# Optimization experiments

Measured on AMD Instinct MI355X. Metric: run time of the kernel, lower is better.

The kernel has to match this reference:

```python
import jax, jax.numpy as jnp
import numpy as np
from jax import lax

FPS_NUM = 512
GROUP_NUM = 32
RADIUS = 0.2
BIG = 1e10


def setup_inputs() -> dict:
    key = jax.random.key(0)
    k1, k2 = jax.random.split(key)
    B, N = 8, 32768
    xyz = jax.random.normal(k1, (B, N, 3), dtype=jnp.float32)
    farthest_init = jax.random.randint(k2, (B,), 0, N, dtype=jnp.int32)
    return {"xyz": xyz, "farthest_init": farthest_init}


def _fps(xyz, farthest_init):
    # xyz: [B, N, 3] -> centroids [B, FPS_NUM] int32
    B, N, _ = xyz.shape
    batch_ix = jnp.arange(B)

    def step(carry, _):
        distance, farthest = carry          # [B,N], [B]
        centroid = xyz[batch_ix, farthest]  # [B,3]
        dist = jnp.sum((xyz - centroid[:, None, :]) ** 2, axis=-1)  # [B,N]
        distance = jnp.minimum(distance, dist)
        new_farthest = jnp.argmax(distance, axis=1).astype(farthest.dtype)
        return (distance, new_farthest), farthest

    init = (jnp.full((B, N), BIG, dtype=xyz.dtype), farthest_init)
    _, centroids_t = lax.scan(step, init, None, length=FPS_NUM)  # [FPS_NUM, B]
    return centroids_t.T  # [B, FPS_NUM]


def _ball_query(xyz, centroids_xyz):
    # xyz [B,N,3], centroids_xyz [B,S,3] -> idx [B,S,GROUP_NUM]
    # Pairwise squared distances: [B, S, N]
    dist = jnp.sum((xyz[:, None, :, :] - centroids_xyz[:, :, None, :]) ** 2, axis=-1)
    dist = jnp.where(dist > RADIUS ** 2, BIG, dist)
    idx = jnp.argsort(dist, axis=-1)[:, :, :GROUP_NUM]
    return idx


def reference(xyz, farthest_init):
    centroids = _fps(xyz, farthest_init)                              # [B, S]
    centroids_xyz = jnp.take_along_axis(xyz, centroids[:, :, None], axis=1)  # [B, S, 3]
    group_idx = _ball_query(xyz, centroids_xyz)                       # [B, S, G]
    # gather grouped points per batch: xyz[b][group_idx[b]] -> [B, S, G, 3]
    grouped_xyz = jax.vmap(lambda pts, ix: pts[ix])(xyz, group_idx)
    relative_xyz = grouped_xyz - centroids_xyz[:, :, None, :]
    combined_points = jnp.concatenate(
        [centroids_xyz[:, :, None, :], relative_xyz], axis=2)         # [B, S, G+1, 3]
    return combined_points, centroids_xyz
```

## Files before the change

kernel.cpp:

```cpp
#include <hip/hip_runtime.h>
#include <stdint.h>

#define NPTS   32768
#define NBATCH 8
#define NFPS   512
#define NGRP   32
#define BIGF   1e10f
#define R2F    0.04f
#define CAP    512
#define QPB    4

#define P      8
#define PPB    (NPTS / P)
#define CHUNKS (PPB / 4)
#define THR    512
#define CPT    (CHUNKS / THR)
#define SLOTB  32
#define FROUNDS 10

typedef unsigned long long u64;
typedef unsigned int v4u __attribute__((ext_vector_type(4)));
typedef unsigned int v2u __attribute__((ext_vector_type(2)));

__device__ __forceinline__ u64 shfl_xor_u64(u64 v, int off) {
    unsigned lo = (unsigned)v, hi = (unsigned)(v >> 32);
    lo = __shfl_xor(lo, off, 64);
    hi = __shfl_xor(hi, off, 64);
    return ((u64)hi << 32) | lo;
}

__device__ __forceinline__ bool msg_valid(v4u A, v2u B) {
    return ((A.y >> 31) == 0) && (A.x >= 0xFFFF8000u) && (B.x == A.x);
}

__device__ __forceinline__ void mail_store(u64 addr, v4u A, v2u B) {
    asm volatile(
        "global_store_dwordx4 %0, %2, off sc0 sc1\n\t"
        "global_store_dwordx2 %1, %3, off sc0 sc1"
        :: "v"(addr), "v"(addr + 16), "v"(A), "v"(B) : "memory");
}

__device__ __forceinline__ void mail_loadF(u64 addr, v4u* A, v2u* B) {
    asm volatile(
        "global_load_dwordx4 %0, %2, off sc0\n\t"
        "global_load_dwordx2 %1, %3, off sc0\n\t"
        "s_waitcnt vmcnt(0)"
        : "=v"(*A), "=v"(*B) : "v"(addr), "v"(addr + 16) : "memory");
}

__device__ __forceinline__ void mail_loadS(u64 addr, v4u* A, v2u* B) {
    asm volatile(
        "global_load_dwordx4 %0, %2, off sc0 sc1\n\t"
        "global_load_dwordx2 %1, %3, off sc0 sc1\n\t"
        "s_waitcnt vmcnt(0)"
        : "=v"(*A), "=v"(*B) : "v"(addr), "v"(addr + 16) : "memory");
}

__global__ __launch_bounds__(THR) void fps_kernel(
    const float* __restrict__ xyz,
    const int* __restrict__ finit,
    int* __restrict__ cidx,
    u64 mailAddr)
{
#pragma clang fp contract(off)
    const int gb = blockIdx.x;
    const int b  = gb & 7;
    const int me = gb >> 3;
    const int t  = threadIdx.x;
    const float* __restrict__ base = xyz + (size_t)b * (NPTS * 3);

    __shared__ float4 xs4[CHUNKS], ys4[CHUNKS], zs4[CHUNKS];
    __shared__ u64 redK[8];
    __shared__ int farbox;
    __shared__ float cxbox, cybox, czbox;

    float dist[4 * CPT];
#pragma unroll
    for (int j = 0; j < CPT; ++j) {
        const int c = t + j * THR;
        const float4* __restrict__ g4 =
            reinterpret_cast<const float4*>(base) + 3 * (me * CHUNKS + c);
        const float4 q0 = g4[0];
        const float4 q1 = g4[1];
        const float4 q2 = g4[2];
        xs4[c] = make_float4(q0.x, q0.w, q1.z, q2.y);
        ys4[c] = make_float4(q0.y, q1.x, q1.w, q2.z);
        zs4[c] = make_float4(q0.z, q1.y, q2.x, q2.w);
        dist[4 * j + 0] = BIGF; dist[4 * j + 1] = BIGF;
        dist[4 * j + 2] = BIGF; dist[4 * j + 3] = BIGF;
    }

    int far = finit[b];
    float cx = base[3 * far + 0];
    float cy = base[3 * far + 1];
    float cz = base[3 * far + 2];

    const int wid  = t >> 6;
    const int lane = t & 63;

    for (int it = 0; it < NFPS; ++it) {
        if (me == 0 && t == 0) cidx[b * NFPS + it] = far;
        if (it == NFPS - 1) break;

        float vmax = -1.0f;
        int   amax = 0;

#define PROC(K, PX, PY, PZ, GI)                               \
        {                                                     \
            float dx = (PX) - cx;                             \
            float dy = (PY) - cy;                             \
            float dz = (PZ) - cz;                             \
            float d  = dx * dx + dy * dy;                     \
            d = d + dz * dz;                                  \
            float dk = fminf(dist[K], d);                     \
            dist[K] = dk;                                     \
            if (dk > vmax) { vmax = dk; amax = (GI); }        \
        }

#pragma unroll
        for (int j = 0; j < CPT; ++j) {
            const int c  = t + j * THR;
            const float4 xv = xs4[c];
            const float4 yv = ys4[c];
            const float4 zv = zs4[c];
            const int gi = me * PPB + 4 * c;
            PROC(4 * j + 0, xv.x, yv.x, zv.x, gi + 0);
            PROC(4 * j + 1, xv.y, yv.y, zv.y, gi + 1);
            PROC(4 * j + 2, xv.z, yv.z, zv.z, gi + 2);
            PROC(4 * j + 3, xv.w, yv.w, zv.w, gi + 3);
        }
#undef PROC

        u64 key = ((u64)__float_as_uint(vmax) << 32)
                | (unsigned)(0xFFFFFFFFu - (unsigned)amax);
#pragma unroll
        for (int off = 32; off >= 1; off >>= 1) {
            u64 o = shfl_xor_u64(key, off);
            key = (o > key) ? o : key;
        }
        if (lane == 0) redK[wid] = key;
        __syncthreads();

        if (wid == 0) {
            u64 blockKey = redK[0];
#pragma unroll
            for (int w = 1; w < 8; ++w) {
                u64 o = redK[w];
                blockKey = (o > blockKey) ? o : blockKey;
            }
            const int gidx = (int)(0xFFFFFFFFu - (unsigned)(blockKey & 0xFFFFFFFFull));
            const int li   = gidx - me * PPB;
            const float candX = reinterpret_cast<const float*>(xs4)[li];
            const float candY = reinterpret_cast<const float*>(ys4)[li];
            const float candZ = reinterpret_cast<const float*>(zs4)[li];

            const u64 slotRow = mailAddr + (u64)((it * NBATCH + b) * P) * SLOTB;
            if (lane == 0) {
                v4u A; v2u B;
                A.x = (unsigned)(blockKey & 0xFFFFFFFFull);
                A.y = (unsigned)(blockKey >> 32);
                A.z = __float_as_uint(candX);
                A.w = __float_as_uint(candY);
                B.x = A.x;
                B.y = __float_as_uint(candZ);
                mail_store(slotRow + (u64)me * SLOTB, A, B);
            }

            u64   k  = 0;
            float px = candX, py = candY, pz = candZ;
            if (lane < P) {
                if (lane == me) {
                    k = blockKey;
                } else {
                    const u64 a = slotRow + (u64)lane * SLOTB;
                    v4u A; v2u B;
                    int fr = FROUNDS;
                    for (;;) {
                        if (fr > 0) { mail_loadF(a, &A, &B); --fr; }
                        else        { mail_loadS(a, &A, &B); }
                        if (msg_valid(A, B)) break;
                    }
                    k  = ((u64)A.y << 32) | A.x;
                    px = __uint_as_float(A.z);
                    py = __uint_as_float(A.w);
                    pz = __uint_as_float(B.y);
                }
            }
#pragma unroll
            for (int off = 4; off >= 1; off >>= 1) {
                const u64   ok = shfl_xor_u64(k, off);
                const float ox = __shfl_xor(px, off, 64);
                const float oy = __shfl_xor(py, off, 64);
                const float oz = __shfl_xor(pz, off, 64);
                if (ok > k) { k = ok; px = ox; py = oy; pz = oz; }
            }
            if (lane == 0) {
                farbox = (int)(0xFFFFFFFFu - (unsigned)(k & 0xFFFFFFFFull));
                cxbox = px; cybox = py; czbox = pz;
            }
        }
        __syncthreads();
        far = farbox;
        cx = cxbox; cy = cybox; cz = czbox;
    }
}

__global__ __launch_bounds__(256) void ballq_kernel(
    const float* __restrict__ xyz,
    const int* __restrict__ cidx,
    float* __restrict__ out0,
    float* __restrict__ out1)
{
#pragma clang fp contract(off)
    const int blk0 = blockIdx.x * QPB;
    const int b    = blk0 >> 9;
    const int t    = threadIdx.x;
    const float* __restrict__ base = xyz + (size_t)b * (NPTS * 3);

    __shared__ u64 list[QPB][CAP];
    __shared__ int scnt[QPB];
    __shared__ u64 mask0[QPB];
    __shared__ int selIdx[QPB][NGRP];

    if (t < QPB) scnt[t] = 0;

    float cxs[QPB], cys[QPB], czs[QPB];
#pragma unroll
    for (int q = 0; q < QPB; ++q) {
        const int ci = cidx[blk0 + q];
        cxs[q] = base[3 * ci + 0];
        cys[q] = base[3 * ci + 1];
        czs[q] = base[3 * ci + 2];
    }
    __syncthreads();

    if (t < 64) {
        const float px = base[3 * t + 0];
        const float py = base[3 * t + 1];
        const float pz = base[3 * t + 2];
#pragma unroll
        for (int q = 0; q < QPB; ++q) {
            float dx = px - cxs[q];
            float dy = py - cys[q];
            float dz = pz - czs[q];
            float d  = dx * dx + dy * dy;
            d = d + dz * dz;
            u64 mk = __ballot(d <= R2F);
            if (t == 0) mask0[q] = mk;
        }
    }

    for (int k = 0; k < NPTS / 256; ++k) {
        const int p = k * 256 + t;
        const float px = base[3 * p + 0];
        const float py = base[3 * p + 1];
        const float pz = base[3 * p + 2];
#pragma unroll
        for (int q = 0; q < QPB; ++q) {
            float dx = px - cxs[q];
            float dy = py - cys[q];
            float dz = pz - czs[q];
            float d  = dx * dx + dy * dy;
            d = d + dz * dz;
            if (d <= R2F) {
                int pos = atomicAdd(&scnt[q], 1);
                if (pos < CAP)
                    list[q][pos] = (((u64)__float_as_uint(d)) << 32)
                                   | (unsigned)p;
            }
        }
    }
    __syncthreads();

    {
        const int q    = t >> 6;
        const int lane = t & 63;
        const int m = min(scnt[q], CAP);
        for (int j = lane; j < m; j += 64) {
            const u64 kj = list[q][j];
            int rank = 0;
            for (int i = 0; i < m; ++i) rank += (list[q][i] < kj) ? 1 : 0;
            if (rank < NGRP) selIdx[q][rank] = (int)(kj & 0xffffffffu);
        }
    }
    __syncthreads();

    if (t < 33 * QPB) {
        const int q    = t / 33;
        const int slot = t % 33;
        const int sg   = blk0 + q;
        const float cx = cxs[q], cy = cys[q], cz = czs[q];
        const size_t o0 = (size_t)sg * 33 * 3;
        if (slot == 32) {
            out0[o0 + 0] = cx; out0[o0 + 1] = cy; out0[o0 + 2] = cz;
            const size_t o1 = (size_t)sg * 3;
            out1[o1 + 0] = cx; out1[o1 + 1] = cy; out1[o1 + 2] = cz;
        } else {
            const int m = min(scnt[q], CAP);
            const int K = min(m, NGRP);
            int idx;
            if (slot < K) {
                idx = selIdx[q][slot];
            } else {
                u64 zeros = ~mask0[q];
                const int need = slot - K;
                for (int z = 0; z < need; ++z) zeros &= zeros - 1;
                idx = __builtin_ctzll(zeros);
            }
            const float px = base[3 * idx + 0];
            const float py = base[3 * idx + 1];
            const float pz = base[3 * idx + 2];
            out0[o0 + (size_t)(1 + slot) * 3 + 0] = px - cx;
            out0[o0 + (size_t)(1 + slot) * 3 + 1] = py - cy;
            out0[o0 + (size_t)(1 + slot) * 3 + 2] = pz - cz;
        }
    }
}

extern "C" void kernel_launch(void* const* d_in, const int* in_sizes, int n_in,
                              void* d_out, int out_size, void* d_ws, size_t ws_size,
                              hipStream_t stream) {
    const float* xyz   = (const float*)d_in[0];
    const int*   finit = (const int*)d_in[1];
    float* out0 = (float*)d_out;
    float* out1 = out0 + (size_t)NBATCH * NFPS * 33 * 3;

    int* cidx = (int*)d_ws;
    u64  mailAddr = (u64)(uintptr_t)((char*)d_ws
                   + (size_t)NBATCH * NFPS * sizeof(int));

    fps_kernel<<<NBATCH * P, THR, 0, stream>>>(xyz, finit, cidx, mailAddr);
    ballq_kernel<<<(NBATCH * NFPS) / QPB, 256, 0, stream>>>(xyz, cidx, out0, out1);
}
```

Measured before the change: 1.393 ms.

## Replace block barrier reduction with per-wave global mailbox exchange ring

Each wavefront now publishes its local argmax candidate directly to a global mailbox slot, giving 64 slots across the 8 blocks of a batch. Every wave then polls all 64 slots and reduces them itself, which removes both __syncthreads per iteration and the shared-memory block reduction. The mailbox becomes an 8-entry ring, with the iteration number tagged into the key's low bits so stale entries are rejected instead of needing fresh slots per iteration. The cost is more global polling traffic per wave and a 15-bit index/17-bit iteration packing that constrains N and iteration count.

```diff
diff --git a/kernel.cpp b/kernel.cpp
--- a/kernel.cpp
+++ b/kernel.cpp
@@ -15,8 +15,10 @@
 #define CHUNKS (PPB / 4)
 #define THR    512
 #define CPT    (CHUNKS / THR)
+#define NSLOT  64
 #define SLOTB  32
-#define FROUNDS 10
+#define RING   8
+#define FROUNDS 4
 
 typedef unsigned long long u64;
 typedef unsigned int v4u __attribute__((ext_vector_type(4)));
@@ -29,17 +31,12 @@
     return ((u64)hi << 32) | lo;
 }
 
-__device__ __forceinline__ bool msg_valid(v4u A, v2u B) {
-    return ((A.y >> 31) == 0) && (A.x >= 0xFFFF8000u) && (B.x == A.x);
-}
-
 __device__ __forceinline__ void mail_store(u64 addr, v4u A, v2u B) {
     asm volatile(
         "global_store_dwordx4 %0, %2, off sc0 sc1\n\t"
         "global_store_dwordx2 %1, %3, off sc0 sc1"
         :: "v"(addr), "v"(addr + 16), "v"(A), "v"(B) : "memory");
 }
-
 __device__ __forceinline__ void mail_loadF(u64 addr, v4u* A, v2u* B) {
     asm volatile(
         "global_load_dwordx4 %0, %2, off sc0\n\t"
@@ -47,7 +44,6 @@
         "s_waitcnt vmcnt(0)"
         : "=v"(*A), "=v"(*B) : "v"(addr), "v"(addr + 16) : "memory");
 }
-
 __device__ __forceinline__ void mail_loadS(u64 addr, v4u* A, v2u* B) {
     asm volatile(
         "global_load_dwordx4 %0, %2, off sc0 sc1\n\t"
@@ -70,9 +66,6 @@
     const float* __restrict__ base = xyz + (size_t)b * (NPTS * 3);
 
     __shared__ float4 xs4[CHUNKS], ys4[CHUNKS], zs4[CHUNKS];
-    __shared__ u64 redK[8];
-    __shared__ int farbox;
-    __shared__ float cxbox, cybox, czbox;
 
     float dist[4 * CPT];
 #pragma unroll
@@ -97,6 +90,7 @@
 
     const int wid  = t >> 6;
     const int lane = t & 63;
+    const int slotIdx = me * 8 + wid;
 
     for (int it = 0; it < NFPS; ++it) {
         if (me == 0 && t == 0) cidx[b * NFPS + it] = far;
@@ -131,77 +125,61 @@
         }
 #undef PROC
 
-        u64 key = ((u64)__float_as_uint(vmax) << 32)
-                | (unsigned)(0xFFFFFFFFu - (unsigned)amax);
+        const unsigned low = ((unsigned)it << 15)
+                           | (unsigned)(0x7FFF - amax);
+        u64 key = ((u64)__float_as_uint(vmax) << 32) | low;
 #pragma unroll
         for (int off = 32; off >= 1; off >>= 1) {
             u64 o = shfl_xor_u64(key, off);
             key = (o > key) ? o : key;
         }
-        if (lane == 0) redK[wid] = key;
-        __syncthreads();
-
-        if (wid == 0) {
-            u64 blockKey = redK[0];
-#pragma unroll
-            for (int w = 1; w < 8; ++w) {
-                u64 o = redK[w];
-                blockKey = (o > blockKey) ? o : blockKey;
+
+        const u64 rowAddr = mailAddr
+            + (u64)(((it & (RING - 1)) * NBATCH + b) * NSLOT) * SLOTB;
+
+        if (lane == 0) {
+            const int widx = 0x7FFF - (int)(key & 0x7FFF);
+            const int li   = widx - me * PPB;
+            v4u A; v2u B;
+            A.x = (unsigned)(key & 0xFFFFFFFFull);
+            A.y = (unsigned)(key >> 32);
+            A.z = __float_as_uint(reinterpret_cast<const float*>(xs4)[li]);
+            A.w = __float_as_uint(reinterpret_cast<const float*>(ys4)[li]);
+            B.x = A.x;
+            B.y = __float_as_uint(reinterpret_cast<const float*>(zs4)[li]);
+            mail_store(rowAddr + (u64)slotIdx * SLOTB, A, B);
+        }
+
+        const u64 myAddr = rowAddr + (u64)lane * SLOTB;
+        v4u A; v2u B;
+        bool have = false;
+        int  fr = FROUNDS;
+        for (;;) {
+            if (!have) {
+                if (fr > 0) mail_loadF(myAddr, &A, &B);
+                else        mail_loadS(myAddr, &A, &B);
+                have = ((A.x >> 15) == (unsigned)it)
+                     && (B.x == A.x)
+                     && ((A.y >> 31) == 0);
             }
-            const int gidx = (int)(0xFFFFFFFFu - (unsigned)(blockKey & 0xFFFFFFFFull));
-            const int li   = gidx - me * PPB;
-            const float candX = reinterpret_cast<const float*>(xs4)[li];
-            const float candY = reinterpret_cast<const float*>(ys4)[li];
-            const float candZ = reinterpret_cast<const float*>(zs4)[li];
-
-            const u64 slotRow = mailAddr + (u64)((it * NBATCH + b) * P) * SLOTB;
-            if (lane == 0) {
-                v4u A; v2u B;
-                A.x = (unsigned)(blockKey & 0xFFFFFFFFull);
-                A.y = (unsigned)(blockKey >> 32);
-                A.z = __float_as_uint(candX);
-                A.w = __float_as_uint(candY);
-                B.x = A.x;
-                B.y = __float_as_uint(candZ);
-                mail_store(slotRow + (u64)me * SLOTB, A, B);
-            }
-
-            u64   k  = 0;
-            float px = candX, py = candY, pz = candZ;
-            if (lane < P) {
-                if (lane == me) {
-                    k = blockKey;
-                } else {
-                    const u64 a = slotRow + (u64)lane * SLOTB;
-                    v4u A; v2u B;
-                    int fr = FROUNDS;
-                    for (;;) {
-                        if (fr > 0) { mail_loadF(a, &A, &B); --fr; }
-                        else        { mail_loadS(a, &A, &B); }
-                        if (msg_valid(A, B)) break;
-                    }
-                    k  = ((u64)A.y << 32) | A.x;
-                    px = __uint_as_float(A.z);
-                    py = __uint_as_float(A.w);
-                    pz = __uint_as_float(B.y);
-                }
-            }
-#pragma unroll
-            for (int off = 4; off >= 1; off >>= 1) {
-                const u64   ok = shfl_xor_u64(k, off);
-                const float ox = __shfl_xor(px, off, 64);
-                const float oy = __shfl_xor(py, off, 64);
-                const float oz = __shfl_xor(pz, off, 64);
-                if (ok > k) { k = ok; px = ox; py = oy; pz = oz; }
-            }
-            if (lane == 0) {
-                farbox = (int)(0xFFFFFFFFu - (unsigned)(k & 0xFFFFFFFFull));
-                cxbox = px; cybox = py; czbox = pz;
-            }
-        }
-        __syncthreads();
-        far = farbox;
-        cx = cxbox; cy = cybox; cz = czbox;
+            --fr;
+            if (__all(have ? 1 : 0)) break;
+        }
+
+        u64   k  = ((u64)A.y << 32) | A.x;
+        float px = __uint_as_float(A.z);
+        float py = __uint_as_float(A.w);
+        float pz = __uint_as_float(B.y);
+#pragma unroll
+        for (int off = 32; off >= 1; off >>= 1) {
+            const u64   ok = shfl_xor_u64(k, off);
+            const float ox = __shfl_xor(px, off, 64);
+            const float oy = __shfl_xor(py, off, 64);
+            const float oz = __shfl_xor(pz, off, 64);
+            if (ok > k) { k = ok; px = ox; py = oy; pz = oz; }
+        }
+        far = 0x7FFF - (int)(k & 0x7FFF);
+        cx = px; cy = py; cz = pz;
     }
 }
 
```

New measurement: 2.220 ms. +59.4%, slower.

## Double FPS block width to 1024 threads and batch 8 queries per ball-query block

Applied to the files above, without the earlier changes.

The FPS kernel now runs 1024 threads per block, so each thread handles one float4 chunk and the block reduction spans 16 waves. The two-phase mailbox polling (relaxed loads first, then system-scope loads) becomes a single system-scope load loop. The ball-query kernel processes 8 centroids per block with strided loops, halving the block count. Wider FPS blocks aim to cut per-iteration latency, but the 16-wave reduction is longer and the stronger polling loads may add latency.

```diff
diff --git a/kernel.cpp b/kernel.cpp
--- a/kernel.cpp
+++ b/kernel.cpp
@@ -8,15 +8,13 @@
 #define BIGF   1e10f
 #define R2F    0.04f
 #define CAP    512
-#define QPB    4
+#define QPB    8
 
 #define P      8
 #define PPB    (NPTS / P)
 #define CHUNKS (PPB / 4)
-#define THR    512
-#define CPT    (CHUNKS / THR)
+#define THR    1024
 #define SLOTB  32
-#define FROUNDS 10
 
 typedef unsigned long long u64;
 typedef unsigned int v4u __attribute__((ext_vector_type(4)));
@@ -39,16 +37,7 @@
         "global_store_dwordx2 %1, %3, off sc0 sc1"
         :: "v"(addr), "v"(addr + 16), "v"(A), "v"(B) : "memory");
 }
-
-__device__ __forceinline__ void mail_loadF(u64 addr, v4u* A, v2u* B) {
-    asm volatile(
-        "global_load_dwordx4 %0, %2, off sc0\n\t"
-        "global_load_dwordx2 %1, %3, off sc0\n\t"
-        "s_waitcnt vmcnt(0)"
-        : "=v"(*A), "=v"(*B) : "v"(addr), "v"(addr + 16) : "memory");
-}
-
-__device__ __forceinline__ void mail_loadS(u64 addr, v4u* A, v2u* B) {
+__device__ __forceinline__ void mail_load(u64 addr, v4u* A, v2u* B) {
     asm volatile(
         "global_load_dwordx4 %0, %2, off sc0 sc1\n\t"
         "global_load_dwordx2 %1, %3, off sc0 sc1\n\t"
@@ -70,14 +59,13 @@
     const float* __restrict__ base = xyz + (size_t)b * (NPTS * 3);
 
     __shared__ float4 xs4[CHUNKS], ys4[CHUNKS], zs4[CHUNKS];
-    __shared__ u64 redK[8];
+    __shared__ u64 redK[16];
     __shared__ int farbox;
     __shared__ float cxbox, cybox, czbox;
 
-    float dist[4 * CPT];
-#pragma unroll
-    for (int j = 0; j < CPT; ++j) {
-        const int c = t + j * THR;
+    float dist[4];
+    {
+        const int c = t;
         const float4* __restrict__ g4 =
             reinterpret_cast<const float4*>(base) + 3 * (me * CHUNKS + c);
         const float4 q0 = g4[0];
@@ -86,8 +74,7 @@
         xs4[c] = make_float4(q0.x, q0.w, q1.z, q2.y);
         ys4[c] = make_float4(q0.y, q1.x, q1.w, q2.z);
         zs4[c] = make_float4(q0.z, q1.y, q2.x, q2.w);
-        dist[4 * j + 0] = BIGF; dist[4 * j + 1] = BIGF;
-        dist[4 * j + 2] = BIGF; dist[4 * j + 3] = BIGF;
+        dist[0] = BIGF; dist[1] = BIGF; dist[2] = BIGF; dist[3] = BIGF;
     }
 
     int far = finit[b];
@@ -116,18 +103,16 @@
             dist[K] = dk;                                     \
             if (dk > vmax) { vmax = dk; amax = (GI); }        \
         }
-
-#pragma unroll
-        for (int j = 0; j < CPT; ++j) {
-            const int c  = t + j * THR;
+        {
+            const int c  = t;
             const float4 xv = xs4[c];
             const float4 yv = ys4[c];
             const float4 zv = zs4[c];
             const int gi = me * PPB + 4 * c;
-            PROC(4 * j + 0, xv.x, yv.x, zv.x, gi + 0);
-            PROC(4 * j + 1, xv.y, yv.y, zv.y, gi + 1);
-            PROC(4 * j + 2, xv.z, yv.z, zv.z, gi + 2);
-            PROC(4 * j + 3, xv.w, yv.w, zv.w, gi + 3);
+            PROC(0, xv.x, yv.x, zv.x, gi + 0);
+            PROC(1, xv.y, yv.y, zv.y, gi + 1);
+            PROC(2, xv.z, yv.z, zv.z, gi + 2);
+            PROC(3, xv.w, yv.w, zv.w, gi + 3);
         }
 #undef PROC
 
@@ -144,7 +129,7 @@
         if (wid == 0) {
             u64 blockKey = redK[0];
 #pragma unroll
-            for (int w = 1; w < 8; ++w) {
+            for (int w = 1; w < 16; ++w) {
                 u64 o = redK[w];
                 blockKey = (o > blockKey) ? o : blockKey;
             }
@@ -174,10 +159,8 @@
                 } else {
                     const u64 a = slotRow + (u64)lane * SLOTB;
                     v4u A; v2u B;
-                    int fr = FROUNDS;
                     for (;;) {
-                        if (fr > 0) { mail_loadF(a, &A, &B); --fr; }
-                        else        { mail_loadS(a, &A, &B); }
+                        mail_load(a, &A, &B);
                         if (msg_valid(A, B)) break;
                     }
                     k  = ((u64)A.y << 32) | A.x;
@@ -273,21 +256,22 @@
     __syncthreads();
 
     {
-        const int q    = t >> 6;
         const int lane = t & 63;
-        const int m = min(scnt[q], CAP);
-        for (int j = lane; j < m; j += 64) {
-            const u64 kj = list[q][j];
-            int rank = 0;
-            for (int i = 0; i < m; ++i) rank += (list[q][i] < kj) ? 1 : 0;
-            if (rank < NGRP) selIdx[q][rank] = (int)(kj & 0xffffffffu);
+        for (int q = t >> 6; q < QPB; q += 4) {
+            const int m = min(scnt[q], CAP);
+            for (int j = lane; j < m; j += 64) {
+                const u64 kj = list[q][j];
+                int rank = 0;
+                for (int i = 0; i < m; ++i) rank += (list[q][i] < kj) ? 1 : 0;
+                if (rank < NGRP) selIdx[q][rank] = (int)(kj & 0xffffffffu);
+            }
         }
     }
     __syncthreads();
 
-    if (t < 33 * QPB) {
-        const int q    = t / 33;
-        const int slot = t % 33;
+    for (int s = t; s < 33 * QPB; s += 256) {
+        const int q    = s / 33;
+        const int slot = s % 33;
         const int sg   = blk0 + q;
         const float cx = cxs[q], cy = cys[q], cz = czs[q];
         const size_t o0 = (size_t)sg * 33 * 3;
```

Result: faster. 1.270 ms (-8.8%).
